# Optimization experiments

Hardware: AMD Instinct MI355X
Metric: run time of the kernel (lower is better)

Reference implementation:

```python
import jax, jax.numpy as jnp
import numpy as np

B, T, DIM, HEADS, DH = 4, 2048, 1024, 16, 64
MAX_SEQ_LEN = 2048


def setup_inputs() -> dict:
    key = jax.random.key(0)
    k1, k2, k3, k4 = jax.random.split(key, 4)
    x = jax.random.normal(k1, (B, T, DIM), dtype=jnp.float32)
    W_qkv = jax.random.normal(k2, (DIM, 3 * HEADS * DH), dtype=jnp.float32) * (DIM ** -0.5)
    W_0 = jax.random.normal(k3, (HEADS * DH, DIM), dtype=jnp.float32) * ((HEADS * DH) ** -0.5)
    rel_bias = jax.random.normal(k4, (2 * MAX_SEQ_LEN - 1, HEADS), dtype=jnp.float32) * 0.02
    return {"x": x, "W_qkv": W_qkv, "W_0": W_0, "rel_bias": rel_bias}


def reference(x, W_qkv, W_0, rel_bias):
    b, t, dim = x.shape
    heads = rel_bias.shape[1]
    dh = W_qkv.shape[1] // (3 * heads)
    scale = dh ** -0.5

    qkv = x @ W_qkv  # (b, t, 3*heads*dh), feature layout is (d, k, h): d slowest, h fastest
    qkv = qkv.reshape(b, t, dh, 3, heads)
    qkv = jnp.transpose(qkv, (3, 0, 4, 1, 2))  # (3, b, h, t, d)
    q, k, v = qkv[0], qkv[1], qkv[2]

    scores = jnp.einsum('bhid,bhjd->bhij', q, k) * scale  # (b, h, t, t)

    causal = jnp.tril(jnp.ones((t, t), dtype=bool))
    scores = jnp.where(causal[None, None], scores, -jnp.inf)

    # relative position bias: index = j - i + t - 1
    rel_idx = jnp.arange(t)[None, :] - jnp.arange(t)[:, None] + (t - 1)  # (t, t)
    bias = rel_bias[rel_idx]  # (t, t, heads)
    scores = scores + jnp.transpose(bias, (2, 0, 1))[None]

    attn = jax.nn.softmax(scores, axis=-1)
    out = jnp.einsum('bhij,bhjd->bhid', attn, v)  # (b, h, t, d)
    out = jnp.transpose(out, (0, 2, 1, 3)).reshape(b, t, heads * dh)
    return out @ W_0
```

## Files before the change

kernel.cpp:

```cpp
#include <hip/hip_runtime.h>
#include <hip/hip_bf16.h>
#include <stdint.h>

#define B_ 4
#define T_ 2048
#define NH 16
#define DH 64
#define DIM 1024
#define NF 3072
#define QKS 2048

typedef unsigned short u16;
typedef uint32_t u32;
typedef __bf16 bf16;
typedef bf16 bf16x8 __attribute__((ext_vector_type(8)));
typedef float f32x4 __attribute__((ext_vector_type(4)));
typedef u16 u16x8 __attribute__((ext_vector_type(8)));
typedef u16 u16x4 __attribute__((ext_vector_type(4)));

__device__ __forceinline__ u16 f2bf(float f) {
    u32 u = __builtin_bit_cast(u32, f);
    u = (u + 0x7fffu + ((u >> 16) & 1u)) >> 16;
    return (u16)u;
}

__device__ __forceinline__ float exp2f_fast(float x) {
#if __has_builtin(__builtin_amdgcn_exp2f)
    return __builtin_amdgcn_exp2f(x);
#else
    return exp2f(x);
#endif
}

#define GLOAD16(g, l)                                                          \
    __builtin_amdgcn_global_load_lds(                                          \
        (const __attribute__((address_space(1))) u32*)(g),                     \
        (__attribute__((address_space(3))) u32*)(l), 16, 0, 0)


__global__ __launch_bounds__(256) void cvt_bf16_k(const float* __restrict__ src,
                                                  u16* __restrict__ dst, int n8) {
    int i = blockIdx.x * 256 + threadIdx.x;
    if (i >= n8) return;
    const float4* s = (const float4*)src + (size_t)i * 2;
    float4 a = s[0], b = s[1];
    u16x8 o;
    o[0]=f2bf(a.x); o[1]=f2bf(a.y); o[2]=f2bf(a.z); o[3]=f2bf(a.w);
    o[4]=f2bf(b.x); o[5]=f2bf(b.y); o[6]=f2bf(b.z); o[7]=f2bf(b.w);
    *(u16x8*)(dst + (size_t)i * 8) = o;
}

template <int PERM>
__global__ __launch_bounds__(256) void wcvt_t_k(const float* __restrict__ src,
                                                u16* __restrict__ dst, int K, int N) {
    __shared__ float tile[32][33];
    int n0 = blockIdx.x * 32, k0 = blockIdx.y * 32;
    int c = threadIdx.x & 31, r0 = threadIdx.x >> 5;
#pragma unroll
    for (int i = 0; i < 4; i++) {
        int r = r0 + i * 8;
        tile[r][c] = src[(size_t)(k0 + r) * N + n0 + c];
    }
    __syncthreads();
#pragma unroll
    for (int i = 0; i < 4; i++) {
        int r = r0 + i * 8;
        int n = n0 + r;
        int nd;
        if (PERM) {
            int d = n / 48, rem = n - d * 48;
            int kk = rem >> 4, h = rem & 15;
            nd = kk * 1024 + h * 64 + d;
        } else {
            nd = n;
        }
        dst[(size_t)nd * K + k0 + c] = f2bf(tile[c][r]);
    }
}

__global__ __launch_bounds__(256) void rbt_k(const float* __restrict__ rb,
                                             u16* __restrict__ rbT2,
                                             u16* __restrict__ rbT2s) {
    int i = blockIdx.x * 256 + threadIdx.x;
    if (i >= NH * 4096) return;
    int h = i >> 12, d = i & 4095;
    float v = (d <= 2047) ? rb[(size_t)d * NH + h] * 1.44269504f : -1e30f;
    rbT2[i] = __builtin_bit_cast(u16, (bf16)v);
    int d2 = d + 1;
    float v2 = (d2 <= 2047) ? rb[(size_t)d2 * NH + h] * 1.44269504f : -1e30f;
    rbT2s[i] = __builtin_bit_cast(u16, (bf16)v2);
}


template <int OUTMODE>
__global__ __launch_bounds__(256, 2) void gemm_bt_k(const u16* __restrict__ A,
                                                    const u16* __restrict__ Bt,
                                                    void* __restrict__ Cout,
                                                    u16* __restrict__ Vt,
                                                    int M, int N, int K) {
    __shared__ __align__(16) u16 As[128 * 64];
    __shared__ __align__(16) u16 Bs[128 * 64];
    const int tid = threadIdx.x;
    const int wave = tid >> 6, lane = tid & 63;
    const int bm = blockIdx.x, bn = blockIdx.y;
    const int wr = (wave >> 1) * 64, wc = (wave & 1) * 64;
    const int lrow = lane & 15, g4 = lane >> 4;
    const int srow8 = lane >> 3;
    const int scs = (lane & 7) ^ srow8;
    const u16* Ab = A + (size_t)(bm * 128 + wave * 32) * K;
    const u16* Bb = Bt + (size_t)(bn * 128 + wave * 32) * K;
    u16* AsW = As + wave * 2048;
    u16* BsW = Bs + wave * 2048;
    const bool vt = (OUTMODE == 1) && (bn >= 16);
    f32x4 acc[4][4] = {};

    for (int k0 = 0; k0 < K; k0 += 64) {
        __syncthreads();
#pragma unroll
        for (int g = 0; g < 4; g++) {
            GLOAD16(Ab + (size_t)(g * 8 + srow8) * K + k0 + scs * 8, AsW + g * 512);
            GLOAD16(Bb + (size_t)(g * 8 + srow8) * K + k0 + scs * 8, BsW + g * 512);
        }
        __syncthreads();
#pragma unroll
        for (int kk2 = 0; kk2 < 2; kk2++) {
            bf16x8 af[4], bfr[4];
#pragma unroll
            for (int i = 0; i < 4; i++)
                af[i] = *(const bf16x8*)&As[(wr + i * 16 + lrow) * 64 +
                                            (((kk2 * 4 + g4) ^ (lrow & 7)) * 8)];
#pragma unroll
            for (int j = 0; j < 4; j++)
                bfr[j] = *(const bf16x8*)&Bs[(wc + j * 16 + lrow) * 64 +
                                             (((kk2 * 4 + g4) ^ (lrow & 7)) * 8)];
            if (vt) {
#pragma unroll
                for (int i = 0; i < 4; i++)
#pragma unroll
                    for (int j = 0; j < 4; j++)
                        acc[i][j] = __builtin_amdgcn_mfma_f32_16x16x32_bf16(
                            bfr[j], af[i], acc[i][j], 0, 0, 0);
            } else {
#pragma unroll
                for (int i = 0; i < 4; i++)
#pragma unroll
                    for (int j = 0; j < 4; j++)
                        acc[i][j] = __builtin_amdgcn_mfma_f32_16x16x32_bf16(
                            af[i], bfr[j], acc[i][j], 0, 0, 0);
            }
        }
    }

    const int crow = (lane >> 4) * 4, ccol = lane & 15;
    if (vt) {
#pragma unroll
        for (int i = 0; i < 4; i++)
#pragma unroll
            for (int j = 0; j < 4; j++) {
                int gm = bm * 128 + wr + i * 16 + ccol;
                int b = gm >> 11, tt = gm & 2047;
#pragma unroll
                for (int r = 0; r < 4; r++) {
                    int f = (bn - 16) * 128 + wc + j * 16 + crow + r;
                    int h = f >> 6, d = f & 63;
                    Vt[(((size_t)(b * NH + h)) * DH + d) * T_ + tt] =
                        f2bf(acc[i][j][r]);
                }
            }
    } else {
#pragma unroll
        for (int i = 0; i < 4; i++)
#pragma unroll
            for (int j = 0; j < 4; j++) {
                int gm = bm * 128 + wr + i * 16 + crow;
                int gn = bn * 128 + wc + j * 16 + ccol;
#pragma unroll
                for (int r = 0; r < 4; r++) {
                    if (OUTMODE == 1)
                        ((u16*)Cout)[(size_t)(gm + r) * N + gn] = f2bf(acc[i][j][r]);
                    else
                        ((float*)Cout)[(size_t)(gm + r) * N + gn] = acc[i][j][r];
                }
            }
    }
}

__global__ __launch_bounds__(256, 2) void flash_attn_k(const u16* __restrict__ qkF,
                                                       const u16* __restrict__ Vt,
                                                       const u16* __restrict__ rbT2,
                                                       const u16* __restrict__ rbT2s,
                                                       u16* __restrict__ O) {
    __shared__ __align__(16) u16 Ks[2][64 * 64];
    __shared__ __align__(16) u16 Vs[2][64 * 64];
    __shared__ __align__(16) u16 Ps[4][2][16 * 64];
    __shared__ __align__(16) u16 rbs2a[4096];
    __shared__ __align__(16) u16 rbs2b[4096];
    const int tid = threadIdx.x, wave = tid >> 6, lane = tid & 63;
    const int Lid = blockIdx.x;
    const int c = Lid & 7, u = Lid >> 3;
    const int bh = ((u & 7) << 3) | c;
    const int pair = u >> 3;
    const int h = bh & 15, b = bh >> 4;
    const int l15 = lane & 15, g4 = lane >> 4;
    const float SC2 = 0.125f * 1.44269504f;

    {
        *(u16x8*)&rbs2a[tid * 8] = *(const u16x8*)&rbT2[(size_t)h * 4096 + tid * 8];
        *(u16x8*)&rbs2a[2048 + tid * 8] = *(const u16x8*)&rbT2[(size_t)h * 4096 + 2048 + tid * 8];
        *(u16x8*)&rbs2b[tid * 8] = *(const u16x8*)&rbT2s[(size_t)h * 4096 + tid * 8];
        *(u16x8*)&rbs2b[2048 + tid * 8] = *(const u16x8*)&rbT2s[(size_t)h * 4096 + 2048 + tid * 8];
    }

    const size_t trow = (size_t)b * T_;
    const int srow = tid >> 2;
    const int sch = tid & 3;
    const int sw = srow & 7;
    u16* pwA = &Ps[wave][0][0];
    u16* pwB = &Ps[wave][1][0];
    const u16* kgb = &qkF[(trow + srow) * QKS + 1024 + h * 64];
    const u16* vgb = &Vt[((size_t)bh * DH + srow) * T_];

    u16x8 kv0 = *(const u16x8*)&kgb[sch * 8];
    u16x8 kv1 = *(const u16x8*)&kgb[(sch + 4) * 8];
    u16x8 vv0 = *(const u16x8*)&vgb[sch * 8];
    u16x8 vv1 = *(const u16x8*)&vgb[(sch + 4) * 8];
    *(u16x8*)&Ks[0][srow * 64 + ((sch ^ sw) * 8)] = kv0;
    *(u16x8*)&Ks[0][srow * 64 + (((sch + 4) ^ sw) * 8)] = kv1;
    *(u16x8*)&Vs[0][srow * 64 + ((sch ^ sw) * 8)] = vv0;
    *(u16x8*)&Vs[0][srow * 64 + (((sch + 4) ^ sw) * 8)] = vv1;
    __syncthreads();
    int cur = 0;

    for (int half = 0; half < 2; half++) {
        const int blk = half ? 15 - pair : pair;
        const int qbA = blk * 128 + wave * 16;
        const int qbB = qbA + 64;
        bf16x8 aqA[2], aqB[2];
        aqA[0] = *(const bf16x8*)&qkF[(trow + qbA + l15) * QKS + h * 64 + g4 * 8];
        aqA[1] = *(const bf16x8*)&qkF[(trow + qbA + l15) * QKS + h * 64 + 32 + g4 * 8];
        aqB[0] = *(const bf16x8*)&qkF[(trow + qbB + l15) * QKS + h * 64 + g4 * 8];
        aqB[1] = *(const bf16x8*)&qkF[(trow + qbB + l15) * QKS + h * 64 + 32 + g4 * 8];

        const int ibA = 2047 - l15 + g4 * 4 - qbA;
        const u32* b32A = (const u32*)((ibA & 1) ? &rbs2b[ibA - 1] : &rbs2a[ibA]);
        const u32* b32B = b32A - 32;

        f32x4 oaccA[4] = {}, oaccB[4] = {};
        float lA = 0.f, lB = 0.f;

        const int jtmax = 2 * blk + 1;
        for (int jt = 0; jt <= jtmax; jt++) {
            const int j0 = jt * 64;
            const int j0n = (jt + 1 <= jtmax) ? (jt + 1) * 64 : (half == 0 ? 0 : -1);
            if (j0n >= 0) {
                const u16* kg = kgb + (size_t)j0n * QKS;
                const u16* vg = vgb + j0n;
                kv0 = *(const u16x8*)&kg[sch * 8];
                kv1 = *(const u16x8*)&kg[(sch + 4) * 8];
                vv0 = *(const u16x8*)&vg[sch * 8];
                vv1 = *(const u16x8*)&vg[(sch + 4) * 8];
            }
            const u16* KsC = &Ks[cur][0];
            const u16* VsC = &Vs[cur][0];
            f32x4 sA[4], sB[4];
#pragma unroll
            for (int ni = 0; ni < 4; ni++) {
                f32x4 z = {};
                sA[ni] = z;
                sB[ni] = z;
            }
            __builtin_amdgcn_s_setprio(1);
#pragma unroll
            for (int ni = 0; ni < 4; ni++) {
                int arow = ni * 16 + l15;
#pragma unroll
                for (int kk = 0; kk < 2; kk++) {
                    int ch = kk * 4 + g4;
                    bf16x8 ak = *(const bf16x8*)&KsC[arow * 64 + ((ch ^ (arow & 7)) * 8)];
                    sA[ni] = __builtin_amdgcn_mfma_f32_16x16x32_bf16(ak, aqA[kk], sA[ni], 0, 0, 0);
                    sB[ni] = __builtin_amdgcn_mfma_f32_16x16x32_bf16(ak, aqB[kk], sB[ni], 0, 0, 0);
                }
            }
            __builtin_amdgcn_s_setprio(0);
            const int jo = j0 >> 1;
            {
                float su = 0.f;
#pragma unroll
                for (int ni = 0; ni < 4; ni++) {
                    u32 w0 = b32A[jo + ni * 8];
                    u32 w1 = b32A[jo + ni * 8 + 1];
                    float e0 = exp2f_fast(fmaf(sA[ni][0], SC2, __builtin_bit_cast(float, w0 << 16)));
                    float e1 = exp2f_fast(fmaf(sA[ni][1], SC2, __builtin_bit_cast(float, w0 & 0xffff0000u)));
                    float e2 = exp2f_fast(fmaf(sA[ni][2], SC2, __builtin_bit_cast(float, w1 << 16)));
                    float e3 = exp2f_fast(fmaf(sA[ni][3], SC2, __builtin_bit_cast(float, w1 & 0xffff0000u)));
                    su += (e0 + e1) + (e2 + e3);
                    u16x4 pk;
                    pk[0] = __builtin_bit_cast(u16, (bf16)e0);
                    pk[1] = __builtin_bit_cast(u16, (bf16)e1);
                    pk[2] = __builtin_bit_cast(u16, (bf16)e2);
                    pk[3] = __builtin_bit_cast(u16, (bf16)e3);
                    int colb = ni * 16 + g4 * 4;
                    int ch = colb >> 3, co = colb & 7;
                    *(u16x4*)&pwA[l15 * 64 + ((ch ^ (l15 & 7)) * 8) + co] = pk;
                }
                su += __shfl_xor(su, 16);
                su += __shfl_xor(su, 32);
                lA += su;
            }
            {
                float su = 0.f;
#pragma unroll
                for (int ni = 0; ni < 4; ni++) {
                    u32 w0 = b32B[jo + ni * 8];
                    u32 w1 = b32B[jo + ni * 8 + 1];
                    float e0 = exp2f_fast(fmaf(sB[ni][0], SC2, __builtin_bit_cast(float, w0 << 16)));
                    float e1 = exp2f_fast(fmaf(sB[ni][1], SC2, __builtin_bit_cast(float, w0 & 0xffff0000u)));
                    float e2 = exp2f_fast(fmaf(sB[ni][2], SC2, __builtin_bit_cast(float, w1 << 16)));
                    float e3 = exp2f_fast(fmaf(sB[ni][3], SC2, __builtin_bit_cast(float, w1 & 0xffff0000u)));
                    su += (e0 + e1) + (e2 + e3);
                    u16x4 pk;
                    pk[0] = __builtin_bit_cast(u16, (bf16)e0);
                    pk[1] = __builtin_bit_cast(u16, (bf16)e1);
                    pk[2] = __builtin_bit_cast(u16, (bf16)e2);
                    pk[3] = __builtin_bit_cast(u16, (bf16)e3);
                    int colb = ni * 16 + g4 * 4;
                    int ch = colb >> 3, co = colb & 7;
                    *(u16x4*)&pwB[l15 * 64 + ((ch ^ (l15 & 7)) * 8) + co] = pk;
                }
                su += __shfl_xor(su, 16);
                su += __shfl_xor(su, 32);
                lB += su;
            }
            bf16x8 bpA[2], bpB[2];
#pragma unroll
            for (int kk = 0; kk < 2; kk++) {
                int ch = kk * 4 + g4;
                int off = l15 * 64 + ((ch ^ (l15 & 7)) * 8);
                bpA[kk] = *(const bf16x8*)&pwA[off];
                bpB[kk] = *(const bf16x8*)&pwB[off];
            }
            __builtin_amdgcn_s_setprio(1);
#pragma unroll
            for (int di = 0; di < 4; di++) {
                int vrow = di * 16 + l15;
#pragma unroll
                for (int kk = 0; kk < 2; kk++) {
                    int ch = kk * 4 + g4;
                    bf16x8 av = *(const bf16x8*)&VsC[vrow * 64 + ((ch ^ (vrow & 7)) * 8)];
                    oaccA[di] = __builtin_amdgcn_mfma_f32_16x16x32_bf16(av, bpA[kk], oaccA[di], 0, 0, 0);
                    oaccB[di] = __builtin_amdgcn_mfma_f32_16x16x32_bf16(av, bpB[kk], oaccB[di], 0, 0, 0);
                }
            }
            __builtin_amdgcn_s_setprio(0);
            if (j0n >= 0) {
                u16* Kn = &Ks[cur ^ 1][0];
                u16* Vn = &Vs[cur ^ 1][0];
                *(u16x8*)&Kn[srow * 64 + ((sch ^ sw) * 8)] = kv0;
                *(u16x8*)&Kn[srow * 64 + (((sch + 4) ^ sw) * 8)] = kv1;
                *(u16x8*)&Vn[srow * 64 + ((sch ^ sw) * 8)] = vv0;
                *(u16x8*)&Vn[srow * 64 + (((sch + 4) ^ sw) * 8)] = vv1;
            }
            __syncthreads();
            cur ^= 1;
        }
        {
            float inv = 1.0f / lA;
            u16* orow = &O[((size_t)b * T_ + qbA + l15) * (NH * DH) + h * DH];
#pragma unroll
            for (int di = 0; di < 4; di++) {
                u16x4 ov;
#pragma unroll
                for (int r = 0; r < 4; r++)
                    ov[r] = __builtin_bit_cast(u16, (bf16)(oaccA[di][r] * inv));
                *(u16x4*)&orow[di * 16 + g4 * 4] = ov;
            }
        }
        {
            float inv = 1.0f / lB;
            u16* orow = &O[((size_t)b * T_ + qbB + l15) * (NH * DH) + h * DH];
#pragma unroll
            for (int di = 0; di < 4; di++) {
                u16x4 ov;
#pragma unroll
                for (int r = 0; r < 4; r++)
                    ov[r] = __builtin_bit_cast(u16, (bf16)(oaccB[di][r] * inv));
                *(u16x4*)&orow[di * 16 + g4 * 4] = ov;
            }
        }
    }
}


extern "C" void kernel_launch(void* const* d_in, const int* in_sizes, int n_in,
                              void* d_out, int out_size, void* d_ws, size_t ws_size,
                              hipStream_t stream) {
    const float* x    = (const float*)d_in[0];
    const float* Wqkv = (const float*)d_in[1];
    const float* W0   = (const float*)d_in[2];
    const float* rb   = (const float*)d_in[3];
    char* ws = (char*)d_ws;

    u16*   xb    = (u16*)(ws + 0);
    u16*   WqkvT = (u16*)(ws + 16777216);
    u16*   W0T   = (u16*)(ws + 23068672);
    u16*   rbT2  = (u16*)(ws + 25165824);
    u16*   rbT2s = (u16*)(ws + 25296896);
    u16*   qkF   = (u16*)(ws + 25427968);
    u16*   attnO = (u16*)(ws + 58982400);
    u16*   Vtb   = (u16*)(ws + 75759616);

    cvt_bf16_k<<<4096, 256, 0, stream>>>(x, xb, (B_ * T_ * DIM) / 8);
    wcvt_t_k<1><<<dim3(NF / 32, DIM / 32), 256, 0, stream>>>(Wqkv, WqkvT, DIM, NF);
    wcvt_t_k<0><<<dim3(DIM / 32, DIM / 32), 256, 0, stream>>>(W0, W0T, DIM, DIM);
    rbt_k<<<(NH * 4096 + 255) / 256, 256, 0, stream>>>(rb, rbT2, rbT2s);

    gemm_bt_k<1><<<dim3((B_ * T_) / 128, NF / 128), 256, 0, stream>>>(
        xb, WqkvT, qkF, Vtb, B_ * T_, QKS, DIM);

    flash_attn_k<<<512, 256, 0, stream>>>(qkF, Vtb, rbT2, rbT2s, attnO);

    gemm_bt_k<0><<<dim3((B_ * T_) / 128, DIM / 128), 256, 0, stream>>>(
        attnO, W0T, d_out, nullptr, B_ * T_, DIM, DIM);
}
```

Before: 167.2 us.

## Stage attention K/V tiles with direct global-to-LDS loads; raise GEMM occupancy

The attention kernel now fills the double-buffered K and V shared-memory tiles with a GLOAD16 macro (apparently direct global-to-LDS loads), replacing the previous register round-trip of loads at loop top and stores at loop bottom. Each wave loads its own 16-row slice, and the XOR swizzle is applied to the global source offset. This removes VGPR staging and the separate ds_write phase, so LDS fills can overlap the MFMA work. Separately, the GEMM launch bounds are raised from 2 to 3 blocks per SM, which may force register spills.

```diff
diff --git a/kernel.cpp b/kernel.cpp
--- a/kernel.cpp
+++ b/kernel.cpp
@@ -93,7 +93,7 @@
 
 
 template <int OUTMODE>
-__global__ __launch_bounds__(256, 2) void gemm_bt_k(const u16* __restrict__ A,
+__global__ __launch_bounds__(256, 3) void gemm_bt_k(const u16* __restrict__ A,
                                                     const u16* __restrict__ Bt,
                                                     void* __restrict__ Cout,
                                                     u16* __restrict__ Vt,
@@ -212,22 +212,24 @@
     }
 
     const size_t trow = (size_t)b * T_;
-    const int srow = tid >> 2;
-    const int sch = tid & 3;
-    const int sw = srow & 7;
     u16* pwA = &Ps[wave][0][0];
     u16* pwB = &Ps[wave][1][0];
-    const u16* kgb = &qkF[(trow + srow) * QKS + 1024 + h * 64];
-    const u16* vgb = &Vt[((size_t)bh * DH + srow) * T_];
-
-    u16x8 kv0 = *(const u16x8*)&kgb[sch * 8];
-    u16x8 kv1 = *(const u16x8*)&kgb[(sch + 4) * 8];
-    u16x8 vv0 = *(const u16x8*)&vgb[sch * 8];
-    u16x8 vv1 = *(const u16x8*)&vgb[(sch + 4) * 8];
-    *(u16x8*)&Ks[0][srow * 64 + ((sch ^ sw) * 8)] = kv0;
-    *(u16x8*)&Ks[0][srow * 64 + (((sch + 4) ^ sw) * 8)] = kv1;
-    *(u16x8*)&Vs[0][srow * 64 + ((sch ^ sw) * 8)] = vv0;
-    *(u16x8*)&Vs[0][srow * 64 + (((sch + 4) ^ sw) * 8)] = vv1;
+    const int lrow8 = lane >> 3, lch = lane & 7;
+    const int swz = lch ^ lrow8;
+    const u16* kg0 = &qkF[(trow + wave * 16 + lrow8) * QKS + 1024 + h * 64 + swz * 8];
+    const u16* kg1 = kg0 + (size_t)8 * QKS;
+    const u16* vg0 = &Vt[((size_t)bh * DH + wave * 16 + lrow8) * T_ + swz * 8];
+    const u16* vg1 = vg0 + (size_t)8 * T_;
+
+#define STAGE_KV(j0n, buf)                                                     \
+    do {                                                                       \
+        GLOAD16(kg0 + (size_t)(j0n) * QKS, &Ks[buf][(wave * 16) * 64]);        \
+        GLOAD16(kg1 + (size_t)(j0n) * QKS, &Ks[buf][(wave * 16 + 8) * 64]);    \
+        GLOAD16(vg0 + (j0n), &Vs[buf][(wave * 16) * 64]);                      \
+        GLOAD16(vg1 + (j0n), &Vs[buf][(wave * 16 + 8) * 64]);                  \
+    } while (0)
+
+    STAGE_KV(0, 0);
     __syncthreads();
     int cur = 0;
 
@@ -252,14 +254,7 @@
         for (int jt = 0; jt <= jtmax; jt++) {
             const int j0 = jt * 64;
             const int j0n = (jt + 1 <= jtmax) ? (jt + 1) * 64 : (half == 0 ? 0 : -1);
-            if (j0n >= 0) {
-                const u16* kg = kgb + (size_t)j0n * QKS;
-                const u16* vg = vgb + j0n;
-                kv0 = *(const u16x8*)&kg[sch * 8];
-                kv1 = *(const u16x8*)&kg[(sch + 4) * 8];
-                vv0 = *(const u16x8*)&vg[sch * 8];
-                vv1 = *(const u16x8*)&vg[(sch + 4) * 8];
-            }
+            if (j0n >= 0) STAGE_KV(j0n, cur ^ 1);
             const u16* KsC = &Ks[cur][0];
             const u16* VsC = &Vs[cur][0];
             f32x4 sA[4], sB[4];
@@ -352,14 +347,6 @@
                 }
             }
             __builtin_amdgcn_s_setprio(0);
-            if (j0n >= 0) {
-                u16* Kn = &Ks[cur ^ 1][0];
-                u16* Vn = &Vs[cur ^ 1][0];
-                *(u16x8*)&Kn[srow * 64 + ((sch ^ sw) * 8)] = kv0;
-                *(u16x8*)&Kn[srow * 64 + (((sch + 4) ^ sw) * 8)] = kv1;
-                *(u16x8*)&Vn[srow * 64 + ((sch ^ sw) * 8)] = vv0;
-                *(u16x8*)&Vn[srow * 64 + (((sch + 4) ^ sw) * 8)] = vv1;
-            }
             __syncthreads();
             cur ^= 1;
         }
@@ -388,6 +375,7 @@
             }
         }
     }
+#undef STAGE_KV
 }
 
 
```

Result: slower. 241.1 us (+44.2%).
